# Optimization experiments

Hardware: AMD Instinct MI355X
Metric: run time of the kernel (lower is better)

Reference implementation:

```python
import jax, jax.numpy as jnp
import numpy as np
import math

N_CELLS = 2048; HC_DIM = 11; HC_NODES = 2048
D = 1024; IN_DIM = 512; L = 2; H = 8; B = 2; HD = D // H
# XOR neighbor table: hypercube scatter-to-neighbor == gather-from-neighbor (involution)
NBR_WALK = jnp.asarray(np.arange(HC_NODES)[:, None] ^ (1 << np.arange(HC_DIM)))  # [Nn, hc_dim]
NB_INJ = min(HC_DIM, 6)
NB_FRUST = min(int(math.log2(N_CELLS)), 10)
FRUST_BITS = jnp.asarray(1 << np.arange(NB_FRUST))
N_MORPH = 48; N_FRUST_SAMPLES = min(N_CELLS, 128)


def _walk_step(amps, coin, x_mean):
    coined = jnp.einsum('ij,njd->nid', coin, amps)              # [Nn,2,D] complex
    new1 = coined[:, 1, :][NBR_WALK].sum(1) / HC_DIM            # XOR neighbor mix
    new = jnp.stack([coined[:, 0, :], new1], axis=1)
    new = new * jnp.exp(1j * (x_mean * 0.1))
    return new / (jnp.sqrt((jnp.abs(new) ** 2).sum()) + 1e-8)


def _inject(cells, amps):
    probs = (jnp.abs(amps) ** 2).sum((1, 2))
    probs = probs / (probs.sum() + 1e-8)
    ph = jnp.angle(amps.sum(1)).mean(-1)                        # [Nn]
    idx = jnp.arange(N_CELLS) % HC_NODES
    p = probs[idx]
    phc = ph[idx] * 0.3
    cells = cells * (0.8 + 0.4 * p)[:, None]
    c, s = jnp.cos(phc)[:, None], jnp.sin(phc)[:, None]
    h1, h2 = cells[:, :D // 2], cells[:, D // 2:]
    rot = jnp.concatenate([h1 * c - h2 * s, h1 * s + h2 * c], axis=1)
    cells = 0.5 * rot + 0.5 * cells
    nbr = idx[:, None] ^ (1 << jnp.arange(NB_INJ))              # [n_cells, 6]
    interf = ((p[:, None] - probs[nbr]) * 0.03).sum(1)
    return cells + interf[:, None]


def _frustration(cells, fsigns):
    # sequential in torch (cells[j] may already be updated for j<i) -> fori_loop
    def body(i, cells):
        j = i ^ FRUST_BITS
        valid = (j < N_CELLS).astype(cells.dtype)
        sign = fsigns[i] * fsigns[j] * valid
        infl = (sign[:, None] * cells[j]).sum(0)
        cnt = valid.sum()
        return cells.at[i].set(0.85 * cells[i] + 0.15 * infl / jnp.maximum(cnt, 1.0))
    return jax.lax.fori_loop(0, N_FRUST_SAMPLES, body, cells)


def _standing_wave(cells, step):
    i = jnp.arange(N_CELLS, dtype=cells.dtype)
    fwd = (step * 0.15) % N_CELLS
    bwd = (N_CELLS - step * 0.15) % N_CELLS
    amp = 1.0 / jnp.cosh((i - fwd) / 2) ** 2 + 1.0 / jnp.cosh((i - bwd) / 2) ** 2
    return cells * (1.0 + 0.03 * amp)[:, None]


def _morphism(cells):
    # torch hs[j] are views, so updates are visible sequentially -> fori_loop
    def body(i, cells):
        ms = jnp.tanh(cells[:N_MORPH] - cells[i]).sum(0) / (N_MORPH - 1)  # tanh(0)=0 handles j==i
        return cells.at[i].set(0.9 * cells[i] + 0.1 * ms)
    return jax.lax.fori_loop(0, N_MORPH, body, cells)


def _faction(cells, step, sync=0.15, debate=0.15, n_f=8):
    fsz = N_CELLS // n_f
    h = cells.reshape(n_f, fsz, D)
    h = (1 - sync) * h + sync * h.mean(1, keepdims=True)
    if step > 5:
        g = h.mean(1).mean(0)
        dc = max(1, fsz // 4)
        h = h.at[:, :dc].set((1 - debate) * h[:, :dc] + debate * g)
    return h.reshape(N_CELLS, D)


def _ln(x, g, b, eps=1e-5):
    mu = x.mean(-1, keepdims=True)
    v = ((x - mu) ** 2).mean(-1, keepdims=True)
    return (x - mu) / jnp.sqrt(v + eps) * g + b


def _update_cells(cells, amp_real, amp_imag, coin_real, coin_imag, fsigns, x, step):
    amps = amp_real + 1j * amp_imag
    coin = coin_real + 1j * coin_imag
    x_mean = x.mean()
    for _ in range(2):  # process() runs walk+inject twice
        amps = _walk_step(amps, coin, x_mean)
        cells = _inject(cells, amps)
    cells = _frustration(cells, fsigns)
    cells = _standing_wave(cells, step)
    if step % 3 == 0:
        cells = _morphism(cells)
    return _faction(cells, step)


def _forward(x, amp_real, amp_imag, coin_real, coin_imag, cell_embeddings, frustration_signs,
             w_in, b_in, attn_in_w, attn_in_b, attn_out_w, attn_out_b, ln_g, ln_b, w_out, b_out, step):
    upd = jax.lax.stop_gradient(_update_cells(
        cell_embeddings, amp_real, amp_imag, coin_real, coin_imag, frustration_signs, x, step))
    # straight-through: torch mutates .data in place, Parameter grad flows through updated values
    cells0 = cell_embeddings + jax.lax.stop_gradient(upd - cell_embeddings)
    x_proj = x @ w_in.T + b_in                                   # [B, D]
    cells = cells0[None] + x_proj[:, None] * 0.1                 # [B, S, D]
    tension = jnp.float32(0.0)
    for l in range(L):
        qkv = cells @ attn_in_w[l].T + attn_in_b[l]
        q, k, v = jnp.split(qkv, 3, axis=-1)
        q = q.reshape(B, N_CELLS, H, HD).transpose(0, 2, 1, 3)
        k = k.reshape(B, N_CELLS, H, HD).transpose(0, 2, 1, 3)
        v = v.reshape(B, N_CELLS, H, HD).transpose(0, 2, 1, 3)
        attn = jax.nn.softmax(jnp.einsum('bhqd,bhkd->bhqk', q, k) / math.sqrt(HD), axis=-1)
        out = jnp.einsum('bhqk,bhkd->bhqd', attn, v).transpose(0, 2, 1, 3).reshape(B, N_CELLS, D)
        out = out @ attn_out_w[l].T + attn_out_b[l]
        cells = _ln(cells + out, ln_g[l], ln_b[l])
        tension = tension + jnp.std(attn.mean(1), ddof=1)        # torch MHA averages heads; std unbiased
    tension = tension / L
    output = cells @ w_out.T + b_out                             # [B, S, IN_DIM]
    return output, tension


def setup_inputs():
    key = jax.random.key(0)
    ks = jax.random.split(key, 12)
    x = jax.random.normal(ks[0], (B, IN_DIM), jnp.float32)
    ar = jax.random.normal(ks[1], (HC_NODES, 2, D), jnp.float32) * 0.1
    ai = jax.random.normal(ks[2], (HC_NODES, 2, D), jnp.float32) * 0.1
    nrm = jnp.sqrt((ar ** 2 + ai ** 2).sum()) + 1e-8
    cells = jax.random.normal(ks[3], (N_CELLS, D), jnp.float32) * 0.1
    perm = jax.random.permutation(ks[4], N_CELLS)
    fsigns = jnp.ones(N_CELLS, jnp.float32).at[perm[:N_CELLS // 2]].set(-1.0)
    s = 1.0 / math.sqrt(D)
    return dict(
        x=x, amp_real=ar / nrm, amp_imag=ai / nrm,
        coin_real=jnp.array([[1.0, 1.0], [1.0, -1.0]], jnp.float32) / math.sqrt(2),
        coin_imag=jnp.zeros((2, 2), jnp.float32),
        cell_embeddings=cells, frustration_signs=fsigns,
        w_in=jax.random.normal(ks[5], (D, IN_DIM), jnp.float32) / math.sqrt(IN_DIM),
        b_in=jnp.zeros(D, jnp.float32),
        attn_in_w=jax.random.normal(ks[6], (L, 3 * D, D), jnp.float32) * s,
        attn_in_b=jnp.zeros((L, 3 * D), jnp.float32),
        attn_out_w=jax.random.normal(ks[7], (L, D, D), jnp.float32) * s,
        attn_out_b=jnp.zeros((L, D), jnp.float32),
        ln_g=jnp.ones((L, D), jnp.float32), ln_b=jnp.zeros((L, D), jnp.float32),
        w_out=jax.random.normal(ks[8], (IN_DIM, D), jnp.float32) * s,
        b_out=jnp.zeros(IN_DIM, jnp.float32),
        step=6)


def reference(x, amp_real, amp_imag, coin_real, coin_imag, cell_embeddings, frustration_signs,
              w_in, b_in, attn_in_w, attn_in_b, attn_out_w, attn_out_b, ln_g, ln_b, w_out, b_out, step):
    return _forward(x, amp_real, amp_imag, coin_real, coin_imag, cell_embeddings, frustration_signs,
                    w_in, b_in, attn_in_w, attn_in_b, attn_out_w, attn_out_b, ln_g, ln_b, w_out, b_out, step)
```

## Files before the change

### kernel.cpp

```cpp
#include <hip/hip_runtime.h>

#define U16 unsigned short

typedef short bf16x8 __attribute__((ext_vector_type(8)));
typedef float f32x4 __attribute__((ext_vector_type(4)));

__device__ __forceinline__ float bfp(const U16* p) { return __uint_as_float(((unsigned)(*p)) << 16); }
__device__ __forceinline__ U16 f2bf(float f) {
  unsigned u = __float_as_uint(f);
  u += 0x7FFFu + ((u >> 16) & 1u);
  return (U16)(u >> 16);
}
__device__ __forceinline__ float ldv(const void* p, long i, bool bf) {
  return bf ? bfp((const U16*)p + i) : ((const float*)p)[i];
}
__device__ __forceinline__ void gload_lds16(const U16* g, U16* l) {
  __builtin_amdgcn_global_load_lds((const __attribute__((address_space(1))) void*)g,
                                   (__attribute__((address_space(3))) void*)l, 16, 0, 0);
}


__global__ __launch_bounds__(256) void init_kernel(const void* __restrict__ x, const U16* __restrict__ lng,
                                                   float* __restrict__ scal) {
  __shared__ float red[256];
  __shared__ int fl;
  int t = threadIdx.x;
  if (t == 0) fl = (lng[0] != 0) ? 1 : 0;
  __syncthreads();
  bool bf = fl != 0;
  float s = 0.f;
  for (int i = t; i < 1024; i += 256) s += ldv(x, i, bf);
  red[t] = s; __syncthreads();
  for (int o = 128; o; o >>= 1) { if (t < o) red[t] += red[t + o]; __syncthreads(); }
  if (t == 0) { scal[0] = red[0] * (1.f / 1024.f); scal[16] = bf ? 1.f : 0.f; }
  else if (t < 64 && t != 16) scal[t] = 0.f;
}

__global__ __launch_bounds__(256) void walk_coined_kernel(const void* __restrict__ arv, const void* __restrict__ aiv,
                                                          float* __restrict__ cr, float* __restrict__ ci,
                                                          const void* __restrict__ coinR, const void* __restrict__ coinI,
                                                          const float* __restrict__ scal, int iter) {
  bool bf = scal[16] != 0.f;
  int id = blockIdx.x * 256 + threadIdx.x;
  int n = id >> 10, d = id & 1023;
  size_t b0 = (size_t)n * 2048 + d;
  float pre = 1.f;
  float a0r, a0i, a1r, a1i;
  if (iter == 0) {
    a0r = ldv(arv, b0, bf); a1r = ldv(arv, b0 + 1024, bf);
    a0i = ldv(aiv, b0, bf); a1i = ldv(aiv, b0 + 1024, bf);
  } else {
    pre = 1.f / (sqrtf(scal[iter]) + 1e-8f);
    const float* ar = (const float*)arv;
    const float* ai = (const float*)aiv;
    a0r = ar[b0]; a1r = ar[b0 + 1024]; a0i = ai[b0]; a1i = ai[b0 + 1024];
  }
  a0r *= pre; a0i *= pre; a1r *= pre; a1i *= pre;
  float c00r = ldv(coinR, 0, bf), c01r = ldv(coinR, 1, bf), c10r = ldv(coinR, 2, bf), c11r = ldv(coinR, 3, bf);
  float c00i = ldv(coinI, 0, bf), c01i = ldv(coinI, 1, bf), c10i = ldv(coinI, 2, bf), c11i = ldv(coinI, 3, bf);
  cr[b0]        = c00r * a0r - c00i * a0i + c01r * a1r - c01i * a1i;
  ci[b0]        = c00r * a0i + c00i * a0r + c01r * a1i + c01i * a1r;
  cr[b0 + 1024] = c10r * a0r - c10i * a0i + c11r * a1r - c11i * a1i;
  ci[b0 + 1024] = c10r * a0i + c10i * a0r + c11r * a1i + c11i * a1r;
}

__global__ __launch_bounds__(256) void walk_new_stats_kernel(const float* __restrict__ cr, const float* __restrict__ ci,
                                                             float* __restrict__ ar, float* __restrict__ ai,
                                                             const float* __restrict__ scal, float* __restrict__ scalw,
                                                             int slot, float* __restrict__ probs, float* __restrict__ ph) {
  __shared__ float r1[256], r2[256];
  int n = blockIdx.x, t = threadIdx.x;
  float th = scal[0] * 0.1f;
  float sn, cs; sincosf(th, &sn, &cs);
  float pacc = 0.f, phacc = 0.f;
  #pragma unroll
  for (int it = 0; it < 4; ++it) {
    int d = t + it * 256;
    size_t b0 = (size_t)n * 2048 + d;
    float n0r = cr[b0], n0i = ci[b0];
    float s1r = 0.f, s1i = 0.f;
    #pragma unroll
    for (int k = 0; k < 11; ++k) {
      size_t j = (size_t)(n ^ (1 << k)) * 2048 + 1024 + d;
      s1r += cr[j]; s1i += ci[j];
    }
    s1r *= (1.f / 11.f); s1i *= (1.f / 11.f);
    float o0r = n0r * cs - n0i * sn, o0i = n0r * sn + n0i * cs;
    float o1r = s1r * cs - s1i * sn, o1i = s1r * sn + s1i * cs;
    ar[b0] = o0r; ai[b0] = o0i; ar[b0 + 1024] = o1r; ai[b0 + 1024] = o1i;
    pacc += o0r * o0r + o0i * o0i + o1r * o1r + o1i * o1i;
    phacc += atan2f(o0i + o1i, o0r + o1r);
  }
  r1[t] = pacc; r2[t] = phacc; __syncthreads();
  for (int o = 128; o; o >>= 1) { if (t < o) { r1[t] += r1[t + o]; r2[t] += r2[t + o]; } __syncthreads(); }
  if (t == 0) { probs[n] = r1[0]; ph[n] = r2[0] * (1.f / 1024.f); atomicAdd(&scalw[slot], r1[0]); }
}

__global__ __launch_bounds__(256) void inject_cells_kernel(const void* __restrict__ cellsIn, float* __restrict__ cells,
                                                           const float* __restrict__ probs,
                                                           const float* __restrict__ ph, const float* __restrict__ scal,
                                                           int wslot, int useRaw) {
  bool bf = scal[16] != 0.f;
  int id = blockIdx.x * 256 + threadIdx.x;
  int c = id >> 9, d = id & 511;
  float invn = 1.f / (sqrtf(scal[wslot]) + 1e-8f);
  float inv2 = invn * invn;
  float denom = 1.f / (scal[wslot] * inv2 + 1e-8f);
  float psc = inv2 * denom;
  float p = probs[c] * psc;
  float interf = 0.f;
  #pragma unroll
  for (int j = 0; j < 6; ++j) interf += (p - probs[c ^ (1 << j)] * psc);
  interf *= 0.03f;
  float scale = 0.8f + 0.4f * p;
  float phc = ph[c] * 0.3f;
  float sn, cs; sincosf(phc, &sn, &cs);
  size_t base = (size_t)c * 1024 + d;
  float h1, h2;
  if (useRaw) { h1 = ldv(cellsIn, base, bf) * scale; h2 = ldv(cellsIn, base + 512, bf) * scale; }
  else        { h1 = cells[base] * scale;            h2 = cells[base + 512] * scale; }
  float r1 = h1 * cs - h2 * sn, r2 = h1 * sn + h2 * cs;
  cells[base]       = 0.5f * (r1 + h1) + interf;
  cells[base + 512] = 0.5f * (r2 + h2) + interf;
}

__global__ __launch_bounds__(64) void frustration_kernel(float* __restrict__ cells, const void* __restrict__ fs,
                                                         const float* __restrict__ scal) {
  bool bf = scal[16] != 0.f;
  int d = blockIdx.x;
  int l = threadIdx.x;
  float s0 = ldv(fs, l, bf);
  float s1 = ldv(fs, l + 64, bf);
  float w0 = s0 * cells[(size_t)l * 1024 + d];
  float w1 = s1 * cells[(size_t)(l + 64) * 1024 + d];
  float stat0 = 0.f, stat1 = 0.f;
  #pragma unroll
  for (int b = 7; b < 10; ++b) {
    int j0 = l ^ (1 << b);
    int j1 = (l + 64) ^ (1 << b);
    stat0 += ldv(fs, j0, bf) * cells[(size_t)j0 * 1024 + d];
    stat1 += ldv(fs, j1, bf) * cells[(size_t)j1 * 1024 + d];
  }
  #pragma unroll
  for (int i = 0; i < 128; ++i) {
    const int hi = i >> 6;
    const int li = i & 63;
    float vsrc = (hi == 0) ? w0 : w1;
    float voth = (hi == 0) ? w1 : w0;
    float acc = __shfl(vsrc, li ^ 1) + __shfl(vsrc, li ^ 2) + __shfl(vsrc, li ^ 4)
              + __shfl(vsrc, li ^ 8) + __shfl(vsrc, li ^ 16) + __shfl(vsrc, li ^ 32)
              + __shfl(voth, li);
    if (l == li) {
      if (hi == 0) w0 = 0.85f * w0 + 0.015f * (acc + stat0);
      else         w1 = 0.85f * w1 + 0.015f * (acc + stat1);
    }
  }
  cells[(size_t)l * 1024 + d]        = s0 * w0;
  cells[(size_t)(l + 64) * 1024 + d] = s1 * w1;
}

__global__ __launch_bounds__(256) void standing_kernel(float* __restrict__ cells, const int* __restrict__ stepp) {
  int id = blockIdx.x * 256 + threadIdx.x;
  int c = id >> 10;
  float st = (float)stepp[0] * 0.15f;
  float fwd = fmodf(st, 2048.f);
  float bwd = fmodf(2048.f - st, 2048.f);
  float fi = (float)c;
  float r1 = 1.f / coshf((fi - fwd) * 0.5f);
  float r2 = 1.f / coshf((fi - bwd) * 0.5f);
  cells[id] *= (1.f + 0.03f * (r1 * r1 + r2 * r2));
}

__global__ __launch_bounds__(64) void morphism_kernel(float* __restrict__ cells, const int* __restrict__ stepp) {
  if (stepp[0] % 3 != 0) return;
  int d = blockIdx.x;
  int l = threadIdx.x;
  float v = 0.f;
  if (l < 48) v = cells[(size_t)l * 1024 + d];
  for (int i = 0; i < 48; ++i) {
    float vi = __shfl(v, i);
    float x = v - vi;
    float e2 = __expf(2.f * x);
    float th = (l < 48) ? (1.f - 2.f / (e2 + 1.f)) : 0.f;
    th += __shfl_xor(th, 1);
    th += __shfl_xor(th, 2);
    th += __shfl_xor(th, 4);
    th += __shfl_xor(th, 8);
    th += __shfl_xor(th, 16);
    th += __shfl_xor(th, 32);
    if (l == i) v = 0.9f * v + (0.1f / 47.f) * th;
  }
  if (l < 48) cells[(size_t)l * 1024 + d] = v;
}

__global__ __launch_bounds__(256) void faction_mean_kernel(const float* __restrict__ cells, float* __restrict__ fmean) {
  int id = blockIdx.x * 256 + threadIdx.x;
  int f = id >> 10, d = id & 1023;
  float s = 0.f;
  for (int r = 0; r < 256; ++r) s += cells[(size_t)((f << 8) + r) * 1024 + d];
  fmean[id] = s * (1.f / 256.f);
}
__global__ __launch_bounds__(256) void faction_apply_kernel(float* __restrict__ cells, const float* __restrict__ fmean,
                                                            const int* __restrict__ stepp) {
  int id = blockIdx.x * 256 + threadIdx.x;
  int c = id >> 10, d = id & 1023;
  int f = c >> 8, r = c & 255;
  float v = 0.85f * cells[id] + 0.15f * fmean[f * 1024 + d];
  if (stepp[0] > 5 && r < 64) {
    float g = 0.f;
    #pragma unroll
    for (int ff = 0; ff < 8; ++ff) g += fmean[ff * 1024 + d];
    v = 0.85f * v + 0.15f * g * 0.125f;
  }
  cells[id] = v;
}

__global__ __launch_bounds__(256) void xproj_kernel(const void* __restrict__ x, const void* __restrict__ w_in,
                                                    const void* __restrict__ b_in, float* __restrict__ xp,
                                                    const float* __restrict__ scal) {
  bool bf = scal[16] != 0.f;
  int id = blockIdx.x * 256 + threadIdx.x;
  int b = id >> 10, o = id & 1023;
  float acc = ldv(b_in, o, bf);
  if (bf) {
    const U16* xr = (const U16*)x + b * 512;
    const U16* wr = (const U16*)w_in + (long)o * 512;
    for (int k = 0; k < 512; ++k) acc += bfp(xr + k) * bfp(wr + k);
  } else {
    const float* xr = (const float*)x + b * 512;
    const float* wr = (const float*)w_in + (long)o * 512;
    for (int k = 0; k < 512; ++k) acc += xr[k] * wr[k];
  }
  xp[id] = acc;
}

__global__ __launch_bounds__(256) void cellsB_kernel(const float* __restrict__ cells, const float* __restrict__ xp,
                                                     float* __restrict__ cellsB, U16* __restrict__ cellsB16) {
  int id = blockIdx.x * 256 + threadIdx.x;
  int b = id >> 21;
  int cd = id & ((1 << 21) - 1);
  int d = id & 1023;
  float v = cells[cd] + 0.1f * xp[(b << 10) + d];
  cellsB[id] = v;
  cellsB16[id] = f2bf(v);
}

__global__ __launch_bounds__(256) void wcvt_kernel(const void* __restrict__ W, long off,
                                                   U16* __restrict__ dst, int n4,
                                                   const float* __restrict__ scal) {
  if (scal[16] != 0.f) return;
  int id = blockIdx.x * 256 + threadIdx.x;
  if (id < n4) {
    const float* src = (const float*)W + off;
    float4 v = *(const float4*)&src[(size_t)id * 4];
    ushort4 o;
    o.x = f2bf(v.x); o.y = f2bf(v.y); o.z = f2bf(v.z); o.w = f2bf(v.w);
    *(ushort4*)&dst[(size_t)id * 4] = o;
  }
}

__global__ __launch_bounds__(256) void mfma_gemm_kernel(const U16* __restrict__ A16,
                                                        const void* __restrict__ Wv, long Woff,
                                                        const U16* __restrict__ W16s,
                                                        const void* __restrict__ biasv, long Boff,
                                                        void* __restrict__ Cout, int N, int mode,
                                                        const float* __restrict__ scal) {
  __shared__ U16 Al[4096];
  __shared__ U16 Wl[4096];
  bool bf = scal[16] != 0.f;
  const int K = 1024;
  int t = threadIdx.x;
  int wv = t >> 6, l = t & 63;
  int n0 = blockIdx.x * 128, m0 = blockIdx.y * 128;
  int wmt = (wv & 1) * 4;
  int wnt = (wv >> 1) * 4;
  const U16* Wb = bf ? (const U16*)Wv + Woff : W16s;

  int fr0 = wv * 2, fr1 = fr0 + 1;
  const U16* asrc0 = A16 + (size_t)(m0 + fr0 * 16 + (l & 15)) * K + (l >> 4) * 8;
  const U16* asrc1 = A16 + (size_t)(m0 + fr1 * 16 + (l & 15)) * K + (l >> 4) * 8;
  const U16* wsrc0 = Wb  + (size_t)(n0 + fr0 * 16 + (l & 15)) * K + (l >> 4) * 8;
  const U16* wsrc1 = Wb  + (size_t)(n0 + fr1 * 16 + (l & 15)) * K + (l >> 4) * 8;
  U16* adst0 = &Al[fr0 * 512];
  U16* adst1 = &Al[fr1 * 512];
  U16* wdst0 = &Wl[fr0 * 512];
  U16* wdst1 = &Wl[fr1 * 512];

  f32x4 acc[4][4];
  #pragma unroll
  for (int i = 0; i < 4; ++i)
    #pragma unroll
    for (int j = 0; j < 4; ++j) acc[i][j] = (f32x4){0.f, 0.f, 0.f, 0.f};

  for (int k0 = 0; k0 < K; k0 += 32) {
    __syncthreads();
    gload_lds16(asrc0 + k0, adst0);
    gload_lds16(asrc1 + k0, adst1);
    gload_lds16(wsrc0 + k0, wdst0);
    gload_lds16(wsrc1 + k0, wdst1);
    __syncthreads();
    bf16x8 afr[4], bfr[4];
    #pragma unroll
    for (int i = 0; i < 4; ++i) afr[i] = *(const bf16x8*)&Al[((wmt + i) * 64 + l) * 8];
    #pragma unroll
    for (int j = 0; j < 4; ++j) bfr[j] = *(const bf16x8*)&Wl[((wnt + j) * 64 + l) * 8];
    #pragma unroll
    for (int i = 0; i < 4; ++i)
      #pragma unroll
      for (int j = 0; j < 4; ++j)
        acc[i][j] = __builtin_amdgcn_mfma_f32_16x16x32_bf16(afr[i], bfr[j], acc[i][j], 0, 0, 0);
  }
  bool outBf = (mode == 1) || (mode == 2 && bf);
  int cl = l & 15, rq = l >> 4;
  #pragma unroll
  for (int j = 0; j < 4; ++j) {
    int n = n0 + (wnt + j) * 16 + cl;
    float bv = ldv(biasv, Boff + n, bf);
    #pragma unroll
    for (int i = 0; i < 4; ++i) {
      int mrow = m0 + (wmt + i) * 16 + rq * 4;
      #pragma unroll
      for (int r = 0; r < 4; ++r) {
        float v = acc[i][j][r] + bv;
        if (outBf) ((U16*)Cout)[(size_t)(mrow + r) * N + n] = f2bf(v);
        else       ((float*)Cout)[(size_t)(mrow + r) * N + n] = v;
      }
    }
  }
}

__global__ __launch_bounds__(256) void pack_kv_kernel(const U16* __restrict__ qkv,
                                                      U16* __restrict__ Kp, U16* __restrict__ Vp) {
  __shared__ U16 tile[64][132];
  int t = threadIdx.x;
  int kc = blockIdx.x, bh = blockIdx.y;
  int b = bh >> 3, h = bh & 7;
  size_t dstB = ((size_t)bh * 32 + kc) * 8192;
  if (blockIdx.z == 0) {
    int w = t >> 6, l = t & 63;
    int l16 = l & 15, quad = l >> 4;
    #pragma unroll
    for (int fi = 0; fi < 4; ++fi) {
      int f = w * 4 + fi;
      int nt = f >> 2, kf = f & 3;
      const U16* src = qkv + ((size_t)(b * 2048 + kc * 64 + nt * 16 + l16)) * 3072 + 1024 + h * 128 + kf * 32 + quad * 8;
      *(uint4*)(Kp + dstB + (size_t)f * 512 + l * 8) = *(const uint4*)src;
    }
  } else {
    int r = t >> 2, c0 = (t & 3) * 32;
    const U16* src = qkv + ((size_t)(b * 2048 + kc * 64 + r)) * 3072 + 2048 + h * 128 + c0;
    #pragma unroll
    for (int q = 0; q < 8; ++q)
      *(ushort4*)&tile[r][c0 + q * 4] = *(const ushort4*)(src + q * 4);
    __syncthreads();
    #pragma unroll
    for (int i = 0; i < 4; ++i) {
      int p = t + 256 * i;
      int g = p >> 6, l = p & 63;
      int l16 = l & 15, quad = l >> 4;
      int nt = g >> 1, kf = g & 1;
      U16 vals[8];
      #pragma unroll
      for (int j = 0; j < 8; ++j) vals[j] = tile[kf * 32 + quad * 8 + j][nt * 16 + l16];
      *(uint4*)(Vp + dstB + (size_t)g * 512 + l * 8) = *(const uint4*)vals;
    }
  }
}

__global__ __launch_bounds__(256) void zero_zg_kernel(float* __restrict__ zg) {
  int id = blockIdx.x * 256 + threadIdx.x;
  if (id < 294912) zg[id] = 0.f;
}

#define EHST 1040
#define EBST (8 * EHST)
__global__ __launch_bounds__(512, 2) void attn_mfma_kernel(U16* __restrict__ qkv,
                                                           const U16* __restrict__ Kp, const U16* __restrict__ Vp,
                                                           float* __restrict__ O32a,
                                                           float* __restrict__ zg) {
  __shared__ U16 ebuf[2 * EBST];
  int t = threadIdx.x;
  int w = t >> 6;
  int l = t & 63;
  int l16 = l & 15, quad = l >> 4;
  int idx = blockIdx.x;
  int khalf = idx & 1;
  int b = (idx >> 1) & 1;
  int q0 = (idx >> 2) * 32;
  size_t rowB = (size_t)b * 2048;
  const float sc = 0.08838834764831845f;
  const int c0 = khalf * 32, cend = c0 + 32;

  bf16x8 afr[2][4];
  #pragma unroll
  for (int s = 0; s < 2; ++s) {
    const U16* Qb = qkv + (rowB + q0 + s * 16 + l16) * 3072 + w * 128 + quad * 8;
    #pragma unroll
    for (int kf = 0; kf < 4; ++kf) afr[s][kf] = *(const bf16x8*)(Qb + kf * 32);
  }

  f32x4 oacc[2][8];
  #pragma unroll
  for (int s = 0; s < 2; ++s)
    #pragma unroll
    for (int i = 0; i < 8; ++i) oacc[s][i] = (f32x4){0.f, 0.f, 0.f, 0.f};
  f32x4 gacc[2];
  gacc[0] = (f32x4){0.f, 0.f, 0.f, 0.f};
  gacc[1] = (f32x4){0.f, 0.f, 0.f, 0.f};
  float zacc[2][4] = {{0.f, 0.f, 0.f, 0.f}, {0.f, 0.f, 0.f, 0.f}};

  const U16* KpB = Kp + (size_t)(b * 8 + w) * 262144;
  const U16* VpB = Vp + (size_t)(b * 8 + w) * 262144;

  bf16x8 bK[2][4];
  bf16x8 bV[8];
  {
    int kc64 = c0 >> 1, nh = (c0 & 1) * 2, vk = c0 & 1;
    #pragma unroll
    for (int i = 0; i < 2; ++i)
      #pragma unroll
      for (int kf = 0; kf < 4; ++kf)
        bK[i][kf] = *(const bf16x8*)(KpB + (size_t)kc64 * 8192 + (size_t)((nh + i) * 4 + kf) * 512 + l * 8);
    #pragma unroll
    for (int nt = 0; nt < 8; ++nt)
      bV[nt] = *(const bf16x8*)(VpB + (size_t)kc64 * 8192 + (size_t)(nt * 2 + vk) * 512 + l * 8);
  }

  for (int c = c0; c < cend; ++c) {
    f32x4 sacc[2][2];
    #pragma unroll
    for (int s = 0; s < 2; ++s)
      #pragma unroll
      for (int i = 0; i < 2; ++i) {
        sacc[s][i] = (f32x4){0.f, 0.f, 0.f, 0.f};
        #pragma unroll
        for (int kf = 0; kf < 4; ++kf)
          sacc[s][i] = __builtin_amdgcn_mfma_f32_16x16x32_bf16(afr[s][kf], bK[i][kf], sacc[s][i], 0, 0, 0);
      }
    U16* eb = &ebuf[(c & 1) * EBST + w * EHST];
    #pragma unroll
    for (int s = 0; s < 2; ++s) {
      #pragma unroll
      for (int i = 0; i < 2; ++i) {
        int kq = i * 2 + (l16 >> 3);
        int j = l16 & 7;
        #pragma unroll
        for (int r = 0; r < 4; ++r) {
          float e = __expf(fminf(sacc[s][i][r] * sc, 30.f));
          zacc[s][r] += e;
          eb[s * 512 + kq * 128 + (quad * 4 + r) * 8 + j] = f2bf(e);
        }
      }
    }
    __syncthreads();
    if (c + 1 < cend) {
      int cn = c + 1, kc64 = cn >> 1, nh = (cn & 1) * 2;
      #pragma unroll
      for (int i = 0; i < 2; ++i)
        #pragma unroll
        for (int kf = 0; kf < 4; ++kf)
          bK[i][kf] = *(const bf16x8*)(KpB + (size_t)kc64 * 8192 + (size_t)((nh + i) * 4 + kf) * 512 + l * 8);
    }
    #pragma unroll
    for (int s = 0; s < 2; ++s) {
      bf16x8 pfr = *(const bf16x8*)&eb[s * 512 + l * 8];
      #pragma unroll
      for (int nt = 0; nt < 8; ++nt)
        oacc[s][nt] = __builtin_amdgcn_mfma_f32_16x16x32_bf16(pfr, bV[nt], oacc[s][nt], 0, 0, 0);
    }
    if (c + 1 < cend) {
      int cn = c + 1, kc64 = cn >> 1, vk = cn & 1;
      #pragma unroll
      for (int nt = 0; nt < 8; ++nt)
        bV[nt] = *(const bf16x8*)(VpB + (size_t)kc64 * 8192 + (size_t)(nt * 2 + vk) * 512 + l * 8);
    }
    {
      const U16* gb = &ebuf[(c & 1) * EBST];
      #pragma unroll
      for (int s = 0; s < 2; ++s) {
        bf16x8 gfr = *(const bf16x8*)(gb + (size_t)(l & 7) * EHST + s * 512
                                      + (quad * 16 + w * 2 + ((l >> 3) & 1)) * 8);
        gacc[s] = __builtin_amdgcn_mfma_f32_16x16x32_bf16(gfr, gfr, gacc[s], 0, 0, 0);
      }
    }
  }
  #pragma unroll
  for (int s = 0; s < 2; ++s)
    #pragma unroll
    for (int r = 0; r < 4; ++r) {
      float z = zacc[s][r];
      z += __shfl_xor(z, 1); z += __shfl_xor(z, 2);
      z += __shfl_xor(z, 4); z += __shfl_xor(z, 8);
      zacc[s][r] = z;
    }
  if (l16 == 0) {
    #pragma unroll
    for (int s = 0; s < 2; ++s)
      #pragma unroll
      for (int r = 0; r < 4; ++r) {
        size_t m = rowB + q0 + s * 16 + quad * 4 + r;
        atomicAdd(&zg[m * 8 + w], zacc[s][r]);
      }
  }
  #pragma unroll
  for (int s = 0; s < 2; ++s)
    #pragma unroll
    for (int r = 0; r < 4; ++r) {
      size_t m = rowB + q0 + s * 16 + quad * 4 + r;
      float* orow;
      if (khalf == 0) orow = O32a + m * 1024 + w * 128 + l16;
      else            orow = (float*)(qkv + m * 3072 + 1024) + w * 128 + l16;
      #pragma unroll
      for (int nt = 0; nt < 8; ++nt) orow[nt * 16] = oacc[s][nt][r];
    }
  {
    int h2 = l16 & 7, b2 = l16 >> 3;
    int a = quad >> 1;
    if (a == b2) {
      float* G = zg + 32768;
      #pragma unroll
      for (int s = 0; s < 2; ++s) {
        size_t m = rowB + q0 + s * 16 + w * 2 + a;
        #pragma unroll
        for (int r = 0; r < 4; ++r) {
          int h1 = (quad * 4 + r) & 7;
          atomicAdd(&G[m * 64 + h1 * 8 + h2], gacc[s][r]);
        }
      }
    }
  }
}

__global__ __launch_bounds__(256) void attn_norm_kernel(const float* __restrict__ O32a, const U16* __restrict__ qkv,
                                                        const float* __restrict__ zg, U16* __restrict__ O16) {
  int id = blockIdx.x * 256 + threadIdx.x;
  int base = id * 4;
  int m = base >> 10, d = base & 1023;
  const float* ob = (const float*)(qkv + (size_t)m * 3072 + 1024);
  float4 a = *(const float4*)&O32a[base];
  float4 bv = *(const float4*)&ob[d];
  float inv = 1.f / zg[m * 8 + (d >> 7)];
  ushort4 o;
  o.x = f2bf((a.x + bv.x) * inv);
  o.y = f2bf((a.y + bv.y) * inv);
  o.z = f2bf((a.z + bv.z) * inv);
  o.w = f2bf((a.w + bv.w) * inv);
  *(ushort4*)&O16[base] = o;
}

__global__ __launch_bounds__(256) void gram_fin_kernel(const float* __restrict__ zg, float* __restrict__ scal, int slot) {
  __shared__ float red[256];
  int t = threadIdx.x;
  const float* G = zg + 32768;
  float s = 0.f;
  for (int i = blockIdx.x * 256 * 16 + t; i < (blockIdx.x + 1) * 256 * 16; i += 256) {
    int m = i >> 6, h1 = (i >> 3) & 7, h2 = i & 7;
    s += G[i] / (zg[m * 8 + h1] * zg[m * 8 + h2]);
  }
  red[t] = s; __syncthreads();
  for (int o = 128; o; o >>= 1) { if (t < o) red[t] += red[t + o]; __syncthreads(); }
  if (t == 0) atomicAdd(&scal[slot], red[0] * (1.f / 64.f) - (blockIdx.x == 0 ? 2.0f : 0.0f));
}

__global__ __launch_bounds__(256) void ln_kernel(float* __restrict__ cellsB, U16* __restrict__ cellsB16,
                                                 const float* __restrict__ proj,
                                                 const void* __restrict__ gv, const void* __restrict__ bv, long off,
                                                 const float* __restrict__ scal) {
  __shared__ float red[256];
  bool bf = scal[16] != 0.f;
  int row = blockIdx.x, t = threadIdx.x;
  size_t base = (size_t)row * 1024;
  int d = 4 * t;
  float4 cv = *(const float4*)&cellsB[base + d];
  float4 pv = *(const float4*)&proj[base + d];
  float v0 = cv.x + pv.x, v1 = cv.y + pv.y, v2 = cv.z + pv.z, v3 = cv.w + pv.w;
  red[t] = v0 + v1 + v2 + v3; __syncthreads();
  for (int o = 128; o; o >>= 1) { if (t < o) red[t] += red[t + o]; __syncthreads(); }
  float mu = red[0] * (1.f / 1024.f);
  __syncthreads();
  float d0 = v0 - mu, d1 = v1 - mu, d2 = v2 - mu, d3 = v3 - mu;
  red[t] = d0 * d0 + d1 * d1 + d2 * d2 + d3 * d3; __syncthreads();
  for (int o = 128; o; o >>= 1) { if (t < o) red[t] += red[t + o]; __syncthreads(); }
  float rstd = rsqrtf(red[0] * (1.f / 1024.f) + 1e-5f);
  float4 out;
  out.x = d0 * rstd * ldv(gv, off + d, bf)     + ldv(bv, off + d, bf);
  out.y = d1 * rstd * ldv(gv, off + d + 1, bf) + ldv(bv, off + d + 1, bf);
  out.z = d2 * rstd * ldv(gv, off + d + 2, bf) + ldv(bv, off + d + 2, bf);
  out.w = d3 * rstd * ldv(gv, off + d + 3, bf) + ldv(bv, off + d + 3, bf);
  *(float4*)&cellsB[base + d] = out;
  ushort4 ob;
  ob.x = f2bf(out.x); ob.y = f2bf(out.y); ob.z = f2bf(out.z); ob.w = f2bf(out.w);
  *(ushort4*)&cellsB16[base + d] = ob;
}

__global__ void tension_kernel(const float* __restrict__ scal, void* __restrict__ out) {
  bool bf = scal[16] != 0.f;
  float cnt = 8388608.f;
  float ten = 0.f;
  for (int l = 0; l < 2; ++l) {
    float v = scal[8 + l] / (cnt - 1.f);
    ten += sqrtf(fmaxf(v, 0.f));
  }
  ten *= 0.5f;
  if (bf) ((U16*)out)[2097152] = f2bf(ten);
  else    ((float*)out)[2097152] = ten;
}

extern "C" void kernel_launch(void* const* d_in, const int* in_sizes, int n_in,
                              void* d_out, int out_size, void* d_ws, size_t ws_size,
                              hipStream_t stream) {
  const void* X    = d_in[0];
  const void* AR   = d_in[1];
  const void* AI   = d_in[2];
  const void* CRc  = d_in[3];
  const void* CIc  = d_in[4];
  const void* CE   = d_in[5];
  const void* FS   = d_in[6];
  const void* WIN  = d_in[7];
  const void* BIN  = d_in[8];
  const void* AIW  = d_in[9];
  const void* AIB  = d_in[10];
  const void* AOW  = d_in[11];
  const void* AOB  = d_in[12];
  const void* LNG  = d_in[13];
  const void* LNB  = d_in[14];
  const void* WOUT = d_in[15];
  const void* BOUT = d_in[16];
  const int* STEP  = (const int*)d_in[17];

  float* ws = (float*)d_ws;
  float* scal  = ws;
  float* probs = ws + 64;
  float* ph    = ws + 64 + 2048;
  float* fmean = ws + 64 + 4096;
  float* xp    = ws + 64 + 12288;
  float* cells = ws + 16384;
  float* CB    = ws + 16384 + 2097152;
  float* ar = CB;
  float* ai = CB + 4194304;
  float* cr = CB + 8388608;
  float* ci = CB + 12582912;
  float* cellsB   = CB;
  U16*   qkv16    = (U16*)(CB + 4194304);
  float* proj     = CB + 4194304;
  float* O32a     = CB + 10485760;
  U16*   cellsB16 = (U16*)(CB + 12582912);
  U16*   Kp       = (U16*)(CB + 14680064);
  U16*   Vp       = (U16*)cells;
  U16*   O16      = Kp;
  float* zg       = (float*)d_out;
  U16*   Wd16     = (U16*)d_out;
  U16*   WOUT16   = (U16*)proj;

  init_kernel<<<1, 256, 0, stream>>>(X, (const U16*)LNG, scal);

  for (int w = 0; w < 2; ++w) {
    if (w == 0) walk_coined_kernel<<<8192, 256, 0, stream>>>(AR, AI, cr, ci, CRc, CIc, scal, 0);
    else        walk_coined_kernel<<<8192, 256, 0, stream>>>(ar, ai, cr, ci, CRc, CIc, scal, 1);
    walk_new_stats_kernel<<<2048, 256, 0, stream>>>(cr, ci, ar, ai, scal, scal, 1 + w, probs, ph);
    inject_cells_kernel<<<4096, 256, 0, stream>>>(w == 0 ? CE : (const void*)cells, cells,
                                                  probs, ph, scal, 1 + w, w == 0 ? 1 : 0);
  }
  frustration_kernel<<<1024, 64, 0, stream>>>(cells, FS, scal);
  standing_kernel<<<8192, 256, 0, stream>>>(cells, STEP);
  morphism_kernel<<<1024, 64, 0, stream>>>(cells, STEP);
  faction_mean_kernel<<<32, 256, 0, stream>>>(cells, fmean);
  faction_apply_kernel<<<8192, 256, 0, stream>>>(cells, fmean, STEP);

  xproj_kernel<<<8, 256, 0, stream>>>(X, WIN, BIN, xp, scal);
  cellsB_kernel<<<16384, 256, 0, stream>>>(cells, xp, cellsB, cellsB16);

  for (int l = 0; l < 2; ++l) {
    wcvt_kernel<<<3072, 256, 0, stream>>>(AIW, (long)l * 3072 * 1024, Wd16, 786432, scal);
    mfma_gemm_kernel<<<dim3(24, 32), 256, 0, stream>>>(cellsB16, AIW, (long)l * 3072 * 1024, Wd16,
                                                       AIB, (long)l * 3072, qkv16, 3072, 1, scal);
    pack_kv_kernel<<<dim3(32, 16, 2), 256, 0, stream>>>(qkv16, Kp, Vp);
    zero_zg_kernel<<<1152, 256, 0, stream>>>(zg);
    attn_mfma_kernel<<<256, 512, 0, stream>>>(qkv16, Kp, Vp, O32a, zg);
    attn_norm_kernel<<<4096, 256, 0, stream>>>(O32a, qkv16, zg, O16);
    gram_fin_kernel<<<64, 256, 0, stream>>>(zg, scal, 8 + l);
    wcvt_kernel<<<1024, 256, 0, stream>>>(AOW, (long)l * 1024 * 1024, Wd16, 262144, scal);
    mfma_gemm_kernel<<<dim3(8, 32), 256, 0, stream>>>(O16, AOW, (long)l * 1024 * 1024, Wd16,
                                                      AOB, (long)l * 1024, proj, 1024, 0, scal);
    ln_kernel<<<4096, 256, 0, stream>>>(cellsB, cellsB16, proj, LNG, LNB, (long)l * 1024, scal);
  }
  wcvt_kernel<<<512, 256, 0, stream>>>(WOUT, 0, WOUT16, 131072, scal);
  mfma_gemm_kernel<<<dim3(4, 32), 256, 0, stream>>>(cellsB16, WOUT, 0, WOUT16,
                                                    BOUT, 0, d_out, 512, 2, scal);
  tension_kernel<<<1, 1, 0, stream>>>(scal, d_out);
}
```

Before: 785.8 us.

## Warp-specialize attention into producer and consumer wave groups

The attention kernel moves from 8 to 16 waves per block. Waves 0-7 compute QK^T scores, exponentials, softmax denominators and the Gram accumulation, producing the next chunk into a double-buffered LDS area. Waves 8-15 consume the previous chunk's probabilities for the PV MMA. This is meant to overlap score and exp work with PV MMAs and split register pressure across waves. The cost is more threads per block, possibly lower block occupancy under launch_bounds(1024,4), and a synchronization scheme that must stay correct across both roles.

```diff
diff --git a/kernel.cpp b/kernel.cpp
--- a/kernel.cpp
+++ b/kernel.cpp
@@ -374,13 +374,14 @@
 
 #define EHST 1040
 #define EBST (8 * EHST)
-__global__ __launch_bounds__(512, 2) void attn_mfma_kernel(U16* __restrict__ qkv,
-                                                           const U16* __restrict__ Kp, const U16* __restrict__ Vp,
-                                                           float* __restrict__ O32a,
-                                                           float* __restrict__ zg) {
+__global__ __launch_bounds__(1024, 4) void attn_mfma_kernel(U16* __restrict__ qkv,
+                                                            const U16* __restrict__ Kp, const U16* __restrict__ Vp,
+                                                            float* __restrict__ O32a,
+                                                            float* __restrict__ zg) {
   __shared__ U16 ebuf[2 * EBST];
   int t = threadIdx.x;
-  int w = t >> 6;
+  int w16 = t >> 6;
+  int h = w16 & 7;
   int l = t & 63;
   int l16 = l & 15, quad = l >> 4;
   int idx = blockIdx.x;
@@ -391,143 +392,149 @@
   const float sc = 0.08838834764831845f;
   const int c0 = khalf * 32, cend = c0 + 32;
 
-  bf16x8 afr[2][4];
-  #pragma unroll
-  for (int s = 0; s < 2; ++s) {
-    const U16* Qb = qkv + (rowB + q0 + s * 16 + l16) * 3072 + w * 128 + quad * 8;
-    #pragma unroll
-    for (int kf = 0; kf < 4; ++kf) afr[s][kf] = *(const bf16x8*)(Qb + kf * 32);
-  }
-
-  f32x4 oacc[2][8];
-  #pragma unroll
-  for (int s = 0; s < 2; ++s)
-    #pragma unroll
-    for (int i = 0; i < 8; ++i) oacc[s][i] = (f32x4){0.f, 0.f, 0.f, 0.f};
-  f32x4 gacc[2];
-  gacc[0] = (f32x4){0.f, 0.f, 0.f, 0.f};
-  gacc[1] = (f32x4){0.f, 0.f, 0.f, 0.f};
-  float zacc[2][4] = {{0.f, 0.f, 0.f, 0.f}, {0.f, 0.f, 0.f, 0.f}};
-
-  const U16* KpB = Kp + (size_t)(b * 8 + w) * 262144;
-  const U16* VpB = Vp + (size_t)(b * 8 + w) * 262144;
-
-  bf16x8 bK[2][4];
-  bf16x8 bV[8];
-  {
-    int kc64 = c0 >> 1, nh = (c0 & 1) * 2, vk = c0 & 1;
-    #pragma unroll
-    for (int i = 0; i < 2; ++i)
-      #pragma unroll
-      for (int kf = 0; kf < 4; ++kf)
-        bK[i][kf] = *(const bf16x8*)(KpB + (size_t)kc64 * 8192 + (size_t)((nh + i) * 4 + kf) * 512 + l * 8);
-    #pragma unroll
-    for (int nt = 0; nt < 8; ++nt)
-      bV[nt] = *(const bf16x8*)(VpB + (size_t)kc64 * 8192 + (size_t)(nt * 2 + vk) * 512 + l * 8);
-  }
-
-  for (int c = c0; c < cend; ++c) {
-    f32x4 sacc[2][2];
-    #pragma unroll
-    for (int s = 0; s < 2; ++s)
-      #pragma unroll
-      for (int i = 0; i < 2; ++i) {
-        sacc[s][i] = (f32x4){0.f, 0.f, 0.f, 0.f};
-        #pragma unroll
-        for (int kf = 0; kf < 4; ++kf)
-          sacc[s][i] = __builtin_amdgcn_mfma_f32_16x16x32_bf16(afr[s][kf], bK[i][kf], sacc[s][i], 0, 0, 0);
-      }
-    U16* eb = &ebuf[(c & 1) * EBST + w * EHST];
+  if (w16 < 8) {
+    const U16* KpB = Kp + (size_t)(b * 8 + h) * 262144;
+    bf16x8 afr[2][4];
     #pragma unroll
     for (int s = 0; s < 2; ++s) {
-      #pragma unroll
-      for (int i = 0; i < 2; ++i) {
-        int kq = i * 2 + (l16 >> 3);
-        int j = l16 & 7;
-        #pragma unroll
-        for (int r = 0; r < 4; ++r) {
-          float e = __expf(fminf(sacc[s][i][r] * sc, 30.f));
-          zacc[s][r] += e;
-          eb[s * 512 + kq * 128 + (quad * 4 + r) * 8 + j] = f2bf(e);
-        }
-      }
-    }
-    __syncthreads();
-    if (c + 1 < cend) {
-      int cn = c + 1, kc64 = cn >> 1, nh = (cn & 1) * 2;
+      const U16* Qb = qkv + (rowB + q0 + s * 16 + l16) * 3072 + h * 128 + quad * 8;
+      #pragma unroll
+      for (int kf = 0; kf < 4; ++kf) afr[s][kf] = *(const bf16x8*)(Qb + kf * 32);
+    }
+    f32x4 gacc[2];
+    gacc[0] = (f32x4){0.f, 0.f, 0.f, 0.f};
+    gacc[1] = (f32x4){0.f, 0.f, 0.f, 0.f};
+    float zacc[2][4] = {{0.f, 0.f, 0.f, 0.f}, {0.f, 0.f, 0.f, 0.f}};
+    bf16x8 bK[2][4];
+
+    auto kload = [&](int c) {
+      int kc64 = c >> 1, nh = (c & 1) * 2;
       #pragma unroll
       for (int i = 0; i < 2; ++i)
         #pragma unroll
         for (int kf = 0; kf < 4; ++kf)
           bK[i][kf] = *(const bf16x8*)(KpB + (size_t)kc64 * 8192 + (size_t)((nh + i) * 4 + kf) * 512 + l * 8);
-    }
-    #pragma unroll
-    for (int s = 0; s < 2; ++s) {
-      bf16x8 pfr = *(const bf16x8*)&eb[s * 512 + l * 8];
-      #pragma unroll
-      for (int nt = 0; nt < 8; ++nt)
-        oacc[s][nt] = __builtin_amdgcn_mfma_f32_16x16x32_bf16(pfr, bV[nt], oacc[s][nt], 0, 0, 0);
-    }
-    if (c + 1 < cend) {
-      int cn = c + 1, kc64 = cn >> 1, vk = cn & 1;
+    };
+    auto produce = [&](int c) {
+      f32x4 sacc[2][2];
+      #pragma unroll
+      for (int s = 0; s < 2; ++s)
+        #pragma unroll
+        for (int i = 0; i < 2; ++i) {
+          sacc[s][i] = (f32x4){0.f, 0.f, 0.f, 0.f};
+          #pragma unroll
+          for (int kf = 0; kf < 4; ++kf)
+            sacc[s][i] = __builtin_amdgcn_mfma_f32_16x16x32_bf16(afr[s][kf], bK[i][kf], sacc[s][i], 0, 0, 0);
+        }
+      U16* eb = &ebuf[(c & 1) * EBST + h * EHST];
+      #pragma unroll
+      for (int s = 0; s < 2; ++s) {
+        #pragma unroll
+        for (int i = 0; i < 2; ++i) {
+          int kq = i * 2 + (l16 >> 3);
+          int j = l16 & 7;
+          #pragma unroll
+          for (int r = 0; r < 4; ++r) {
+            float e = __expf(fminf(sacc[s][i][r] * sc, 30.f));
+            zacc[s][r] += e;
+            eb[s * 512 + kq * 128 + (quad * 4 + r) * 8 + j] = f2bf(e);
+          }
+        }
+      }
+    };
+
+    kload(c0);
+    produce(c0);
+    if (c0 + 1 < cend) kload(c0 + 1);
+
+    for (int c = c0; c < cend; ++c) {
+      __syncthreads();
+      if (c + 1 < cend) {
+        produce(c + 1);
+        if (c + 2 < cend) kload(c + 2);
+      }
+      const U16* gb = &ebuf[(c & 1) * EBST];
+      #pragma unroll
+      for (int s = 0; s < 2; ++s) {
+        bf16x8 gfr = *(const bf16x8*)(gb + (size_t)(l & 7) * EHST + s * 512
+                                      + (quad * 16 + h * 2 + ((l >> 3) & 1)) * 8);
+        gacc[s] = __builtin_amdgcn_mfma_f32_16x16x32_bf16(gfr, gfr, gacc[s], 0, 0, 0);
+      }
+    }
+    #pragma unroll
+    for (int s = 0; s < 2; ++s)
+      #pragma unroll
+      for (int r = 0; r < 4; ++r) {
+        float z = zacc[s][r];
+        z += __shfl_xor(z, 1); z += __shfl_xor(z, 2);
+        z += __shfl_xor(z, 4); z += __shfl_xor(z, 8);
+        zacc[s][r] = z;
+      }
+    if (l16 == 0) {
+      #pragma unroll
+      for (int s = 0; s < 2; ++s)
+        #pragma unroll
+        for (int r = 0; r < 4; ++r) {
+          size_t m = rowB + q0 + s * 16 + quad * 4 + r;
+          atomicAdd(&zg[m * 8 + h], zacc[s][r]);
+        }
+    }
+    {
+      int h2 = l16 & 7, b2 = l16 >> 3;
+      int a = quad >> 1;
+      if (a == b2) {
+        float* G = zg + 32768;
+        #pragma unroll
+        for (int s = 0; s < 2; ++s) {
+          size_t m = rowB + q0 + s * 16 + h * 2 + a;
+          #pragma unroll
+          for (int r = 0; r < 4; ++r) {
+            int h1 = (quad * 4 + r) & 7;
+            atomicAdd(&G[m * 64 + h1 * 8 + h2], gacc[s][r]);
+          }
+        }
+      }
+    }
+  } else {
+    const U16* VpB = Vp + (size_t)(b * 8 + h) * 262144;
+    f32x4 oacc[2][8];
+    #pragma unroll
+    for (int s = 0; s < 2; ++s)
+      #pragma unroll
+      for (int i = 0; i < 8; ++i) oacc[s][i] = (f32x4){0.f, 0.f, 0.f, 0.f};
+    bf16x8 bV[8];
+
+    auto vload = [&](int c) {
+      int kc64 = c >> 1, vk = c & 1;
       #pragma unroll
       for (int nt = 0; nt < 8; ++nt)
         bV[nt] = *(const bf16x8*)(VpB + (size_t)kc64 * 8192 + (size_t)(nt * 2 + vk) * 512 + l * 8);
-    }
-    {
-      const U16* gb = &ebuf[(c & 1) * EBST];
+    };
+
+    vload(c0);
+    for (int c = c0; c < cend; ++c) {
+      __syncthreads();
+      const U16* eb = &ebuf[(c & 1) * EBST + h * EHST];
       #pragma unroll
       for (int s = 0; s < 2; ++s) {
-        bf16x8 gfr = *(const bf16x8*)(gb + (size_t)(l & 7) * EHST + s * 512
-                                      + (quad * 16 + w * 2 + ((l >> 3) & 1)) * 8);
-        gacc[s] = __builtin_amdgcn_mfma_f32_16x16x32_bf16(gfr, gfr, gacc[s], 0, 0, 0);
-      }
-    }
-  }
-  #pragma unroll
-  for (int s = 0; s < 2; ++s)
-    #pragma unroll
-    for (int r = 0; r < 4; ++r) {
-      float z = zacc[s][r];
-      z += __shfl_xor(z, 1); z += __shfl_xor(z, 2);
-      z += __shfl_xor(z, 4); z += __shfl_xor(z, 8);
-      zacc[s][r] = z;
-    }
-  if (l16 == 0) {
+        bf16x8 pfr = *(const bf16x8*)&eb[s * 512 + l * 8];
+        #pragma unroll
+        for (int nt = 0; nt < 8; ++nt)
+          oacc[s][nt] = __builtin_amdgcn_mfma_f32_16x16x32_bf16(pfr, bV[nt], oacc[s][nt], 0, 0, 0);
+      }
+      if (c + 1 < cend) vload(c + 1);
+    }
     #pragma unroll
     for (int s = 0; s < 2; ++s)
       #pragma unroll
       for (int r = 0; r < 4; ++r) {
         size_t m = rowB + q0 + s * 16 + quad * 4 + r;
-        atomicAdd(&zg[m * 8 + w], zacc[s][r]);
-      }
-  }
-  #pragma unroll
-  for (int s = 0; s < 2; ++s)
-    #pragma unroll
-    for (int r = 0; r < 4; ++r) {
-      size_t m = rowB + q0 + s * 16 + quad * 4 + r;
-      float* orow;
-      if (khalf == 0) orow = O32a + m * 1024 + w * 128 + l16;
-      else            orow = (float*)(qkv + m * 3072 + 1024) + w * 128 + l16;
-      #pragma unroll
-      for (int nt = 0; nt < 8; ++nt) orow[nt * 16] = oacc[s][nt][r];
-    }
-  {
-    int h2 = l16 & 7, b2 = l16 >> 3;
-    int a = quad >> 1;
-    if (a == b2) {
-      float* G = zg + 32768;
-      #pragma unroll
-      for (int s = 0; s < 2; ++s) {
-        size_t m = rowB + q0 + s * 16 + w * 2 + a;
+        float* orow;
+        if (khalf == 0) orow = O32a + m * 1024 + h * 128 + l16;
+        else            orow = (float*)(qkv + m * 3072 + 1024) + h * 128 + l16;
         #pragma unroll
-        for (int r = 0; r < 4; ++r) {
-          int h1 = (quad * 4 + r) & 7;
-          atomicAdd(&G[m * 64 + h1 * 8 + h2], gacc[s][r]);
-        }
-      }
-    }
+        for (int nt = 0; nt < 8; ++nt) orow[nt * 16] = oacc[s][nt][r];
+      }
   }
 }
 
@@ -676,7 +683,7 @@
                                                        AIB, (long)l * 3072, qkv16, 3072, 1, scal);
     pack_kv_kernel<<<dim3(32, 16, 2), 256, 0, stream>>>(qkv16, Kp, Vp);
     zero_zg_kernel<<<1152, 256, 0, stream>>>(zg);
-    attn_mfma_kernel<<<256, 512, 0, stream>>>(qkv16, Kp, Vp, O32a, zg);
+    attn_mfma_kernel<<<256, 1024, 0, stream>>>(qkv16, Kp, Vp, O32a, zg);
     attn_norm_kernel<<<4096, 256, 0, stream>>>(O32a, qkv16, zg, O16);
     gram_fin_kernel<<<64, 256, 0, stream>>>(zg, scal, 8 + l);
     wcvt_kernel<<<1024, 256, 0, stream>>>(AOW, (long)l * 1024 * 1024, Wd16, 262144, scal);
```

After: 766.3 us. 2.5% less time.
